# Kernel tuning notes

Measured on AMD Instinct MI355X. Metric: run time of the kernel, lower is better.

The kernel has to match this reference:

```python
import jax, jax.numpy as jnp
import numpy as np

B, L, HP, H, W = 4, 32, 32, 64, 64
D, DFFN, MAXL = 32, 64, 128

def setup_inputs() -> dict:
    key = jax.random.key(0)
    ks = jax.random.split(key, 20)
    rn = lambda k, s, sc=0.1: jax.random.normal(k, s, jnp.float32) * sc
    return {
        'x': jax.random.normal(ks[0], (B, 2 * L * HP, H, W), jnp.float32),
        'in_proj_w': rn(ks[1], (D, 12)), 'in_proj_b': rn(ks[2], (D,)),
        'layer_emb': rn(ks[3], (MAXL, D)),
        'time_decay': rn(ks[4], (D,)), 'time_first': rn(ks[5], (D,)),
        'ln_tm_g': jnp.ones((D,)), 'ln_tm_b': jnp.zeros((D,)),
        'tm_r': rn(ks[6], (D, D)), 'tm_k': rn(ks[7], (D, D)),
        'tm_v': rn(ks[8], (D, D)), 'tm_out': rn(ks[9], (D, D)),
        'ln_cm_g': jnp.ones((D,)), 'ln_cm_b': jnp.zeros((D,)),
        'cm_k': rn(ks[10], (DFFN, D)), 'cm_v': rn(ks[11], (D, DFFN)), 'cm_r': rn(ks[12], (D, D)),
        'gate_w': rn(ks[13], (1, D)), 'gate_b': rn(ks[14], (1,)),
        'row_w': rn(ks[15], (H, D)), 'row_b': rn(ks[16], (H,)),
        'col_w': rn(ks[17], (W, D)), 'col_b': rn(ks[18], (W,)),
    }

def _ln(x, g, b, eps=1e-5):
    mu = x.mean(-1, keepdims=True)
    var = ((x - mu) ** 2).mean(-1, keepdims=True)
    return (x - mu) * jax.lax.rsqrt(var + eps) * g + b

def _stats(a, b):
    # a, b: [B, L, HP, H, W] -> [B, L, HP, 12]
    af = a.reshape(*a.shape[:-2], -1)
    bf = b.reshape(*b.shape[:-2], -1)
    hs = lambda f: jnp.stack([f.mean(-1), f.std(-1, ddof=1), f.min(-1), f.max(-1)], -1)
    d = af - bf
    dm = d.mean(-1, keepdims=True)
    ds = d.std(-1, ddof=1, keepdims=True)
    dl2 = jnp.linalg.norm(d, axis=-1, keepdims=True)
    na = jnp.maximum(jnp.linalg.norm(af, axis=-1), 1e-8)
    nb = jnp.maximum(jnp.linalg.norm(bf, axis=-1), 1e-8)
    cos = ((af * bf).sum(-1) / (na * nb))[..., None]
    return jnp.concatenate([hs(af), hs(bf), dm, ds, dl2, cos], -1)

def reference(x, in_proj_w, in_proj_b, layer_emb, time_decay, time_first,
              ln_tm_g, ln_tm_b, tm_r, tm_k, tm_v, tm_out,
              ln_cm_g, ln_cm_b, cm_k, cm_v, cm_r,
              gate_w, gate_b, row_w, row_b, col_w, col_b):
    n = L * HP
    a = x[:, :n].reshape(B, L, HP, H, W)
    b = x[:, n:].reshape(B, L, HP, H, W)
    stats = _stats(a, b)                                   # [B,L,HP,12]
    feat_in = jnp.einsum('blhs,ds->blhd', stats, in_proj_w) + in_proj_b \
        + layer_emb[:L][None, :, None, :]
    feat_in = jnp.transpose(feat_in, (1, 0, 2, 3))         # [L,B,HP,D]
    wdec = jnp.exp(time_decay)

    def step(state, f):
        aa, bb, pp = state
        xn = _ln(f, ln_tm_g, ln_tm_b)
        r = jax.nn.sigmoid(xn @ tm_r.T)
        k = xn @ tm_k.T
        v = xn @ tm_v.T
        ww = time_first + k
        p = jnp.maximum(pp, ww)
        e1 = jnp.exp(pp - p)
        e2 = jnp.exp(ww - p)
        wkv = (e1 * aa + e2 * v) / jnp.maximum(e1 * bb + e2, 1e-8)
        ww2 = pp - wdec
        p2 = jnp.maximum(ww2, k)
        e1b = jnp.exp(ww2 - p2)
        e2b = jnp.exp(k - p2)
        y = f + r * (wkv @ tm_out.T)
        xn2 = _ln(y, ln_cm_g, ln_cm_b)
        kk = jnp.square(jax.nn.relu(xn2 @ cm_k.T))
        y = y + jax.nn.sigmoid(xn2 @ cm_r.T) * (kk @ cm_v.T)
        return (e1b * aa + e2b * v, e1b * bb + e2b, p2), y

    z = jnp.zeros((B, HP, D), x.dtype)
    init = (z, z, jnp.full((B, HP, D), -1e30, x.dtype))
    _, feats = jax.lax.scan(step, init, feat_in)           # [L,B,HP,D]

    gate = feats @ gate_w.T + gate_b                       # [L,B,HP,1]
    row = feats @ row_w.T + row_b                          # [L,B,HP,H]
    col = feats @ col_w.T + col_b                          # [L,B,HP,W]
    mask = jax.nn.sigmoid(gate[..., None] + row[..., None] + col[..., None, :])
    aT = jnp.transpose(a, (1, 0, 2, 3, 4))
    bT = jnp.transpose(b, (1, 0, 2, 3, 4))
    merged = mask * aT + (1.0 - mask) * bT                 # [L,B,HP,H,W]
    mixed = jnp.transpose(merged, (1, 0, 2, 3, 4)).reshape(B, n, H, W)
    return mixed, jax.nn.sigmoid(gate).mean(), mask.mean()
```

## Files before the change

### kernel.cpp

```cpp
#include <hip/hip_runtime.h>
#include <math.h>


__device__ __forceinline__ float sigf(float v) { return 1.0f / (1.0f + __expf(-v)); }

__global__ __launch_bounds__(256) void k_stats(
    const float* __restrict__ x, const float* __restrict__ in_proj_w,
    const float* __restrict__ in_proj_b, const float* __restrict__ layer_emb,
    const float* __restrict__ ln_tm_g, const float* __restrict__ ln_tm_b,
    const float* __restrict__ tm_r, const float* __restrict__ tm_k,
    const float* __restrict__ tm_v,
    float* __restrict__ f_out, float* __restrict__ r_out,
    float* __restrict__ kv_out)
{
    __shared__ float red[4][9];
    __shared__ float tot[9];
    __shared__ __align__(16) float xn_s[32];
    const int bid = blockIdx.x;
    const int hp = bid & 31, l = (bid >> 5) & 31, bb = bid >> 10;
    const float4* pa = (const float4*)(x + (size_t)(bb * 2048 + l * 32 + hp) * 4096);
    const float4* pb = (const float4*)(x + (size_t)(bb * 2048 + 1024 + l * 32 + hp) * 4096);
    const int t = threadIdx.x;
    const int gidx = ((l * 4 + bb) * 32 + hp) * 32;

    float sa = 0.f, saa = 0.f, sb = 0.f, sbb = 0.f, sab = 0.f;
    float mna = 3.4e38f, mxa = -3.4e38f, mnb = 3.4e38f, mxb = -3.4e38f;
#pragma unroll
    for (int it = 0; it < 4; ++it) {
        float4 a4 = pa[t + it * 256];
        float4 b4 = pb[t + it * 256];
        sa  += a4.x + a4.y + a4.z + a4.w;
        sb  += b4.x + b4.y + b4.z + b4.w;
        saa += a4.x * a4.x + a4.y * a4.y + a4.z * a4.z + a4.w * a4.w;
        sbb += b4.x * b4.x + b4.y * b4.y + b4.z * b4.z + b4.w * b4.w;
        sab += a4.x * b4.x + a4.y * b4.y + a4.z * b4.z + a4.w * b4.w;
        mna = fminf(mna, fminf(fminf(a4.x, a4.y), fminf(a4.z, a4.w)));
        mxa = fmaxf(mxa, fmaxf(fmaxf(a4.x, a4.y), fmaxf(a4.z, a4.w)));
        mnb = fminf(mnb, fminf(fminf(b4.x, b4.y), fminf(b4.z, b4.w)));
        mxb = fmaxf(mxb, fmaxf(fmaxf(b4.x, b4.y), fmaxf(b4.z, b4.w)));
    }
#pragma unroll
    for (int m = 1; m < 64; m <<= 1) {
        sa  += __shfl_xor(sa, m);
        saa += __shfl_xor(saa, m);
        sb  += __shfl_xor(sb, m);
        sbb += __shfl_xor(sbb, m);
        sab += __shfl_xor(sab, m);
        mna = fminf(mna, __shfl_xor(mna, m));
        mxa = fmaxf(mxa, __shfl_xor(mxa, m));
        mnb = fminf(mnb, __shfl_xor(mnb, m));
        mxb = fmaxf(mxb, __shfl_xor(mxb, m));
    }
    const int lane = t & 63, wv = t >> 6;
    if (lane == 0) {
        red[wv][0] = sa;  red[wv][1] = saa; red[wv][2] = sb;  red[wv][3] = sbb;
        red[wv][4] = sab; red[wv][5] = mna; red[wv][6] = mxa; red[wv][7] = mnb;
        red[wv][8] = mxb;
    }
    __syncthreads();
    if (t == 0) {
#pragma unroll
        for (int q = 0; q < 5; ++q) tot[q] = red[0][q] + red[1][q] + red[2][q] + red[3][q];
        tot[5] = fminf(fminf(red[0][5], red[1][5]), fminf(red[2][5], red[3][5]));
        tot[6] = fmaxf(fmaxf(red[0][6], red[1][6]), fmaxf(red[2][6], red[3][6]));
        tot[7] = fminf(fminf(red[0][7], red[1][7]), fminf(red[2][7], red[3][7]));
        tot[8] = fmaxf(fmaxf(red[0][8], red[1][8]), fmaxf(red[2][8], red[3][8]));
    }
    __syncthreads();
    if (t < 32) {
        const float SA = tot[0], SAA = tot[1], SB = tot[2], SBB = tot[3], SAB = tot[4];
        const float inv_n = 1.f / 4096.f, inv_nm1 = 1.f / 4095.f;
        float st[12];
        st[0] = SA * inv_n;
        st[1] = sqrtf(fmaxf(SAA - SA * SA * inv_n, 0.f) * inv_nm1);
        st[2] = tot[5]; st[3] = tot[6];
        st[4] = SB * inv_n;
        st[5] = sqrtf(fmaxf(SBB - SB * SB * inv_n, 0.f) * inv_nm1);
        st[6] = tot[7]; st[7] = tot[8];
        const float SD = SA - SB, SDD = SAA - 2.f * SAB + SBB;
        st[8]  = SD * inv_n;
        st[9]  = sqrtf(fmaxf(SDD - SD * SD * inv_n, 0.f) * inv_nm1);
        st[10] = sqrtf(fmaxf(SDD, 0.f));
        const float na = fmaxf(sqrtf(SAA), 1e-8f), nb2 = fmaxf(sqrtf(SBB), 1e-8f);
        st[11] = SAB / (na * nb2);
        float fv = in_proj_b[t] + layer_emb[l * 32 + t];
#pragma unroll
        for (int s2 = 0; s2 < 12; ++s2) fv += st[s2] * in_proj_w[t * 12 + s2];
        f_out[gidx + t] = fv;
        float s = fv, q = fv * fv;
#pragma unroll
        for (int m = 1; m < 32; m <<= 1) { s += __shfl_xor(s, m, 32); q += __shfl_xor(q, m, 32); }
        const float mu = s * (1.f / 32.f);
        const float var = fmaxf(q * (1.f / 32.f) - mu * mu, 0.f);
        xn_s[t] = (fv - mu) * rsqrtf(var + 1e-5f) * ln_tm_g[t] + ln_tm_b[t];
    }
    __syncthreads();
    if (t < 96) {
        const int d = t & 31;
        const float* wrow = (t < 32 ? tm_r : (t < 64 ? tm_k : tm_v)) + d * 32;
        const float4* w4 = (const float4*)wrow;
        const float4* x4 = (const float4*)xn_s;
        float a0 = 0.f, a1 = 0.f, a2 = 0.f, a3 = 0.f;
#pragma unroll
        for (int jq = 0; jq < 2; ++jq) {
            float4 w, xv;
            w = w4[jq];     xv = x4[jq];     a0 += w.x*xv.x + w.y*xv.y + w.z*xv.z + w.w*xv.w;
            w = w4[jq + 2]; xv = x4[jq + 2]; a1 += w.x*xv.x + w.y*xv.y + w.z*xv.z + w.w*xv.w;
            w = w4[jq + 4]; xv = x4[jq + 4]; a2 += w.x*xv.x + w.y*xv.y + w.z*xv.z + w.w*xv.w;
            w = w4[jq + 6]; xv = x4[jq + 6]; a3 += w.x*xv.x + w.y*xv.y + w.z*xv.z + w.w*xv.w;
        }
        const float dot = (a0 + a1) + (a2 + a3);
        if (t < 32)      r_out[gidx + d] = sigf(dot);
        else if (t < 64) kv_out[2 * (gidx + d)] = dot;
        else             kv_out[2 * (gidx + d) + 1] = dot;
    }
}

__global__ __launch_bounds__(64) void k_wkv(
    const float* __restrict__ kv_in,
    const float* __restrict__ time_decay, const float* __restrict__ time_first,
    float* __restrict__ wkv_out)
{
    const int ch = blockIdx.x * 64 + threadIdx.x;
    const int d = ch & 31;
    const float tf = time_first[d];
    const float wd = __expf(time_decay[d]);
    const float2* kv2 = (const float2*)kv_in;
    float2 kv[32];
#pragma unroll
    for (int l = 0; l < 32; ++l) kv[l] = kv2[l * 4096 + ch];
    float aa = 0.f, bbs = 0.f, pp = -1e30f;
#pragma unroll
    for (int l = 0; l < 32; ++l) {
        const float kc = kv[l].x, vc = kv[l].y;
        const float ww = tf + kc;
        const float p = fmaxf(pp, ww);
        const float e1 = __expf(pp - p), e2 = __expf(ww - p);
        wkv_out[l * 4096 + ch] = (e1 * aa + e2 * vc) / fmaxf(e1 * bbs + e2, 1e-8f);
        const float ww2 = pp - wd;
        const float p2 = fmaxf(ww2, kc);
        const float e1b = __expf(ww2 - p2), e2b = __expf(kc - p2);
        aa = e1b * aa + e2b * vc;
        bbs = e1b * bbs + e2b;
        pp = p2;
    }
}

__global__ __launch_bounds__(256) void k_merge(
    const float* __restrict__ x,
    const float* __restrict__ f_in, const float* __restrict__ r_in,
    const float* __restrict__ wkv_in,
    const float* __restrict__ tm_out,
    const float* __restrict__ ln_cm_g, const float* __restrict__ ln_cm_b,
    const float* __restrict__ cm_k, const float* __restrict__ cm_v,
    const float* __restrict__ cm_r,
    const float* __restrict__ gate_w, const float* __restrict__ gate_b,
    const float* __restrict__ row_w, const float* __restrict__ row_b,
    const float* __restrict__ col_w, const float* __restrict__ col_b,
    float* __restrict__ out, float* __restrict__ gpart, float* __restrict__ mpart)
{
    __shared__ __align__(16) float wkv_s[32];
    __shared__ __align__(16) float xn2_s[32];
    __shared__ __align__(16) float kk_s[64];
    __shared__ __align__(16) float fs[32];
    __shared__ float row_s[64], col_s[64];
    __shared__ float gate_sh;
    __shared__ float red2[4];
    const int bid = blockIdx.x;
    const int hp = bid & 31, l = (bid >> 5) & 31, bb = bid >> 10;
    const int t = threadIdx.x;
    const int gidx = ((l * 4 + bb) * 32 + hp) * 32;

    const float4* pa = (const float4*)(x + (size_t)(bb * 2048 + l * 32 + hp) * 4096);
    const float4* pb = (const float4*)(x + (size_t)(bb * 2048 + 1024 + l * 32 + hp) * 4096);
    float4* po = (float4*)(out + (size_t)(bb * 1024 + l * 32 + hp) * 4096);

    float4 av[4], bv[4];
#pragma unroll
    for (int it = 0; it < 4; ++it) {
        av[it] = pa[t + it * 256];
        bv[it] = pb[t + it * 256];
    }

    if (t < 64) {
        float yv = 0.f, y2 = 0.f;
        if (t < 32) {
            wkv_s[t] = wkv_in[gidx + t];
            const float fv = f_in[gidx + t];
            const float rv = r_in[gidx + t];
            const float4* w4 = (const float4*)(tm_out + t * 32);
            const float4* x4 = (const float4*)wkv_s;
            float a0 = 0.f, a1 = 0.f, a2 = 0.f, a3 = 0.f;
#pragma unroll
            for (int jq = 0; jq < 2; ++jq) {
                float4 w, xv;
                w = w4[jq];     xv = x4[jq];     a0 += w.x*xv.x + w.y*xv.y + w.z*xv.z + w.w*xv.w;
                w = w4[jq + 2]; xv = x4[jq + 2]; a1 += w.x*xv.x + w.y*xv.y + w.z*xv.z + w.w*xv.w;
                w = w4[jq + 4]; xv = x4[jq + 4]; a2 += w.x*xv.x + w.y*xv.y + w.z*xv.z + w.w*xv.w;
                w = w4[jq + 6]; xv = x4[jq + 6]; a3 += w.x*xv.x + w.y*xv.y + w.z*xv.z + w.w*xv.w;
            }
            yv = fv + rv * ((a0 + a1) + (a2 + a3));
            float s = yv, q = yv * yv;
#pragma unroll
            for (int m = 1; m < 32; m <<= 1) { s += __shfl_xor(s, m, 32); q += __shfl_xor(q, m, 32); }
            const float mu = s * (1.f / 32.f);
            const float var = fmaxf(q * (1.f / 32.f) - mu * mu, 0.f);
            xn2_s[t] = (yv - mu) * rsqrtf(var + 1e-5f) * ln_cm_g[t] + ln_cm_b[t];
        }
        {
            const float4* w4 = (const float4*)(cm_k + t * 32);
            const float4* x4 = (const float4*)xn2_s;
            float a0 = 0.f, a1 = 0.f, a2 = 0.f, a3 = 0.f;
#pragma unroll
            for (int jq = 0; jq < 2; ++jq) {
                float4 w, xv;
                w = w4[jq];     xv = x4[jq];     a0 += w.x*xv.x + w.y*xv.y + w.z*xv.z + w.w*xv.w;
                w = w4[jq + 2]; xv = x4[jq + 2]; a1 += w.x*xv.x + w.y*xv.y + w.z*xv.z + w.w*xv.w;
                w = w4[jq + 4]; xv = x4[jq + 4]; a2 += w.x*xv.x + w.y*xv.y + w.z*xv.z + w.w*xv.w;
                w = w4[jq + 6]; xv = x4[jq + 6]; a3 += w.x*xv.x + w.y*xv.y + w.z*xv.z + w.w*xv.w;
            }
            float kk = fmaxf((a0 + a1) + (a2 + a3), 0.f);
            kk_s[t] = kk * kk;
        }
        if (t < 32) {
            float cr;
            {
                const float4* w4 = (const float4*)(cm_r + t * 32);
                const float4* x4 = (const float4*)xn2_s;
                float a0 = 0.f, a1 = 0.f, a2 = 0.f, a3 = 0.f;
#pragma unroll
                for (int jq = 0; jq < 2; ++jq) {
                    float4 w, xv;
                    w = w4[jq];     xv = x4[jq];     a0 += w.x*xv.x + w.y*xv.y + w.z*xv.z + w.w*xv.w;
                    w = w4[jq + 2]; xv = x4[jq + 2]; a1 += w.x*xv.x + w.y*xv.y + w.z*xv.z + w.w*xv.w;
                    w = w4[jq + 4]; xv = x4[jq + 4]; a2 += w.x*xv.x + w.y*xv.y + w.z*xv.z + w.w*xv.w;
                    w = w4[jq + 6]; xv = x4[jq + 6]; a3 += w.x*xv.x + w.y*xv.y + w.z*xv.z + w.w*xv.w;
                }
                cr = sigf((a0 + a1) + (a2 + a3));
            }
            {
                const float4* w4 = (const float4*)(cm_v + t * 64);
                const float4* x4 = (const float4*)kk_s;
                float a0 = 0.f, a1 = 0.f, a2 = 0.f, a3 = 0.f;
#pragma unroll
                for (int jq = 0; jq < 4; ++jq) {
                    float4 w, xv;
                    w = w4[jq];      xv = x4[jq];      a0 += w.x*xv.x + w.y*xv.y + w.z*xv.z + w.w*xv.w;
                    w = w4[jq + 4];  xv = x4[jq + 4];  a1 += w.x*xv.x + w.y*xv.y + w.z*xv.z + w.w*xv.w;
                    w = w4[jq + 8];  xv = x4[jq + 8];  a2 += w.x*xv.x + w.y*xv.y + w.z*xv.z + w.w*xv.w;
                    w = w4[jq + 12]; xv = x4[jq + 12]; a3 += w.x*xv.x + w.y*xv.y + w.z*xv.z + w.w*xv.w;
                }
                y2 = yv + cr * ((a0 + a1) + (a2 + a3));
            }
            fs[t] = y2;
            float g = y2 * gate_w[t];
#pragma unroll
            for (int m = 1; m < 32; m <<= 1) g += __shfl_xor(g, m, 32);
            if (t == 0) gate_sh = g + gate_b[0];
        }
        {
            float a0 = row_b[t], a1 = 0.f, a2 = 0.f, a3 = 0.f;
            float c0 = col_b[t], c1 = 0.f, c2 = 0.f, c3 = 0.f;
#pragma unroll
            for (int d2 = 0; d2 < 8; ++d2) {
                const float f0 = fs[d2], f1 = fs[d2 + 8], f2 = fs[d2 + 16], f3 = fs[d2 + 24];
                a0 += f0 * row_w[t * 32 + d2];
                a1 += f1 * row_w[t * 32 + d2 + 8];
                a2 += f2 * row_w[t * 32 + d2 + 16];
                a3 += f3 * row_w[t * 32 + d2 + 24];
                c0 += f0 * col_w[t * 32 + d2];
                c1 += f1 * col_w[t * 32 + d2 + 8];
                c2 += f2 * col_w[t * 32 + d2 + 16];
                c3 += f3 * col_w[t * 32 + d2 + 24];
            }
            row_s[t] = (a0 + a1) + (a2 + a3);
            col_s[t] = (c0 + c1) + (c2 + c3);
        }
    }
    __syncthreads();

    const float gate = gate_sh;
    float msum = 0.f;
#pragma unroll
    for (int it = 0; it < 4; ++it) {
        const int i = t + it * 256;
        const float4 a4 = av[it];
        const float4 b4 = bv[it];
        const int h = i >> 4, w0 = (i & 15) * 4;
        const float gr = gate + row_s[h];
        const float m0 = sigf(gr + col_s[w0 + 0]);
        const float m1 = sigf(gr + col_s[w0 + 1]);
        const float m2 = sigf(gr + col_s[w0 + 2]);
        const float m3 = sigf(gr + col_s[w0 + 3]);
        float4 o;
        o.x = b4.x + m0 * (a4.x - b4.x);
        o.y = b4.y + m1 * (a4.y - b4.y);
        o.z = b4.z + m2 * (a4.z - b4.z);
        o.w = b4.w + m3 * (a4.w - b4.w);
        po[i] = o;
        msum += m0 + m1 + m2 + m3;
    }
#pragma unroll
    for (int m = 1; m < 64; m <<= 1) msum += __shfl_xor(msum, m);
    if ((t & 63) == 0) red2[t >> 6] = msum;
    __syncthreads();
    if (t == 0) {
        mpart[bid] = red2[0] + red2[1] + red2[2] + red2[3];
        gpart[bid] = sigf(gate);
    }
}

__global__ __launch_bounds__(256) void k_final(
    const float* __restrict__ gpart, const float* __restrict__ mpart,
    float* __restrict__ out)
{
    __shared__ float rg[4], rm[4];
    const int t = threadIdx.x;
    float gs = 0.f, ms = 0.f;
    for (int i = t; i < 4096; i += 256) { gs += gpart[i]; ms += mpart[i]; }
#pragma unroll
    for (int m = 1; m < 64; m <<= 1) { gs += __shfl_xor(gs, m); ms += __shfl_xor(ms, m); }
    if ((t & 63) == 0) { rg[t >> 6] = gs; rm[t >> 6] = ms; }
    __syncthreads();
    if (t == 0) {
        out[16777216] = (rg[0] + rg[1] + rg[2] + rg[3]) * (1.f / 4096.f);
        out[16777217] = (rm[0] + rm[1] + rm[2] + rm[3]) * (1.f / 16777216.f);
    }
}

extern "C" void kernel_launch(void* const* d_in, const int* in_sizes, int n_in,
                              void* d_out, int out_size, void* d_ws, size_t ws_size,
                              hipStream_t stream) {
    const float* x          = (const float*)d_in[0];
    const float* in_proj_w  = (const float*)d_in[1];
    const float* in_proj_b  = (const float*)d_in[2];
    const float* layer_emb  = (const float*)d_in[3];
    const float* time_decay = (const float*)d_in[4];
    const float* time_first = (const float*)d_in[5];
    const float* ln_tm_g    = (const float*)d_in[6];
    const float* ln_tm_b    = (const float*)d_in[7];
    const float* tm_r       = (const float*)d_in[8];
    const float* tm_k       = (const float*)d_in[9];
    const float* tm_v       = (const float*)d_in[10];
    const float* tm_out     = (const float*)d_in[11];
    const float* ln_cm_g    = (const float*)d_in[12];
    const float* ln_cm_b    = (const float*)d_in[13];
    const float* cm_k       = (const float*)d_in[14];
    const float* cm_v       = (const float*)d_in[15];
    const float* cm_r       = (const float*)d_in[16];
    const float* gate_w     = (const float*)d_in[17];
    const float* gate_b     = (const float*)d_in[18];
    const float* row_w      = (const float*)d_in[19];
    const float* row_b      = (const float*)d_in[20];
    const float* col_w      = (const float*)d_in[21];
    const float* col_b      = (const float*)d_in[22];
    float* out = (float*)d_out;

    float* wsf    = (float*)d_ws;
    float* f_ws   = wsf;
    float* r_ws   = wsf + 131072;
    float* kv_ws  = wsf + 262144;
    float* wkv_ws = wsf + 524288;
    float* gpart  = wsf + 655360;
    float* mpart  = wsf + 659456;

    k_stats<<<dim3(4096), dim3(256), 0, stream>>>(
        x, in_proj_w, in_proj_b, layer_emb, ln_tm_g, ln_tm_b,
        tm_r, tm_k, tm_v, f_ws, r_ws, kv_ws);
    k_wkv<<<dim3(64), dim3(64), 0, stream>>>(
        kv_ws, time_decay, time_first, wkv_ws);
    k_merge<<<dim3(4096), dim3(256), 0, stream>>>(
        x, f_ws, r_ws, wkv_ws, tm_out, ln_cm_g, ln_cm_b, cm_k, cm_v, cm_r,
        gate_w, gate_b, row_w, row_b, col_w, col_b, out, gpart, mpart);
    k_final<<<dim3(1), dim3(256), 0, stream>>>(gpart, mpart, out);
}
```

Baseline: 307.4 us.

## Drop a barrier in stats epilogue, add occupancy hints, defer merge loads

```diff
diff --git a/kernel.cpp b/kernel.cpp
--- a/kernel.cpp
+++ b/kernel.cpp
@@ -4,7 +4,7 @@
 
 __device__ __forceinline__ float sigf(float v) { return 1.0f / (1.0f + __expf(-v)); }
 
-__global__ __launch_bounds__(256) void k_stats(
+__global__ __launch_bounds__(256, 4) void k_stats(
     const float* __restrict__ x, const float* __restrict__ in_proj_w,
     const float* __restrict__ in_proj_b, const float* __restrict__ layer_emb,
     const float* __restrict__ ln_tm_g, const float* __restrict__ ln_tm_b,
@@ -14,7 +14,6 @@
     float* __restrict__ kv_out)
 {
     __shared__ float red[4][9];
-    __shared__ float tot[9];
     __shared__ __align__(16) float xn_s[32];
     const int bid = blockIdx.x;
     const int hp = bid & 31, l = (bid >> 5) & 31, bb = bid >> 10;
@@ -58,61 +57,71 @@
         red[wv][8] = mxb;
     }
     __syncthreads();
-    if (t == 0) {
-#pragma unroll
-        for (int q = 0; q < 5; ++q) tot[q] = red[0][q] + red[1][q] + red[2][q] + red[3][q];
-        tot[5] = fminf(fminf(red[0][5], red[1][5]), fminf(red[2][5], red[3][5]));
-        tot[6] = fmaxf(fmaxf(red[0][6], red[1][6]), fmaxf(red[2][6], red[3][6]));
-        tot[7] = fminf(fminf(red[0][7], red[1][7]), fminf(red[2][7], red[3][7]));
-        tot[8] = fmaxf(fmaxf(red[0][8], red[1][8]), fmaxf(red[2][8], red[3][8]));
-    }
-    __syncthreads();
-    if (t < 32) {
-        const float SA = tot[0], SAA = tot[1], SB = tot[2], SBB = tot[3], SAB = tot[4];
-        const float inv_n = 1.f / 4096.f, inv_nm1 = 1.f / 4095.f;
-        float st[12];
-        st[0] = SA * inv_n;
-        st[1] = sqrtf(fmaxf(SAA - SA * SA * inv_n, 0.f) * inv_nm1);
-        st[2] = tot[5]; st[3] = tot[6];
-        st[4] = SB * inv_n;
-        st[5] = sqrtf(fmaxf(SBB - SB * SB * inv_n, 0.f) * inv_nm1);
-        st[6] = tot[7]; st[7] = tot[8];
-        const float SD = SA - SB, SDD = SAA - 2.f * SAB + SBB;
-        st[8]  = SD * inv_n;
-        st[9]  = sqrtf(fmaxf(SDD - SD * SD * inv_n, 0.f) * inv_nm1);
-        st[10] = sqrtf(fmaxf(SDD, 0.f));
-        const float na = fmaxf(sqrtf(SAA), 1e-8f), nb2 = fmaxf(sqrtf(SBB), 1e-8f);
-        st[11] = SAB / (na * nb2);
-        float fv = in_proj_b[t] + layer_emb[l * 32 + t];
-#pragma unroll
-        for (int s2 = 0; s2 < 12; ++s2) fv += st[s2] * in_proj_w[t * 12 + s2];
-        f_out[gidx + t] = fv;
-        float s = fv, q = fv * fv;
-#pragma unroll
-        for (int m = 1; m < 32; m <<= 1) { s += __shfl_xor(s, m, 32); q += __shfl_xor(q, m, 32); }
-        const float mu = s * (1.f / 32.f);
-        const float var = fmaxf(q * (1.f / 32.f) - mu * mu, 0.f);
-        xn_s[t] = (fv - mu) * rsqrtf(var + 1e-5f) * ln_tm_g[t] + ln_tm_b[t];
-    }
-    __syncthreads();
-    if (t < 96) {
+    if (t < 64) {
+        if (t < 32) {
+            const float SA  = red[0][0] + red[1][0] + red[2][0] + red[3][0];
+            const float SAA = red[0][1] + red[1][1] + red[2][1] + red[3][1];
+            const float SB  = red[0][2] + red[1][2] + red[2][2] + red[3][2];
+            const float SBB = red[0][3] + red[1][3] + red[2][3] + red[3][3];
+            const float SAB = red[0][4] + red[1][4] + red[2][4] + red[3][4];
+            const float MNA = fminf(fminf(red[0][5], red[1][5]), fminf(red[2][5], red[3][5]));
+            const float MXA = fmaxf(fmaxf(red[0][6], red[1][6]), fmaxf(red[2][6], red[3][6]));
+            const float MNB = fminf(fminf(red[0][7], red[1][7]), fminf(red[2][7], red[3][7]));
+            const float MXB = fmaxf(fmaxf(red[0][8], red[1][8]), fmaxf(red[2][8], red[3][8]));
+            const float inv_n = 1.f / 4096.f, inv_nm1 = 1.f / 4095.f;
+            float st[12];
+            st[0] = SA * inv_n;
+            st[1] = sqrtf(fmaxf(SAA - SA * SA * inv_n, 0.f) * inv_nm1);
+            st[2] = MNA; st[3] = MXA;
+            st[4] = SB * inv_n;
+            st[5] = sqrtf(fmaxf(SBB - SB * SB * inv_n, 0.f) * inv_nm1);
+            st[6] = MNB; st[7] = MXB;
+            const float SD = SA - SB, SDD = SAA - 2.f * SAB + SBB;
+            st[8]  = SD * inv_n;
+            st[9]  = sqrtf(fmaxf(SDD - SD * SD * inv_n, 0.f) * inv_nm1);
+            st[10] = sqrtf(fmaxf(SDD, 0.f));
+            const float na = fmaxf(sqrtf(SAA), 1e-8f), nb2 = fmaxf(sqrtf(SBB), 1e-8f);
+            st[11] = SAB / (na * nb2);
+            float fv = in_proj_b[t] + layer_emb[l * 32 + t];
+#pragma unroll
+            for (int s2 = 0; s2 < 12; ++s2) fv += st[s2] * in_proj_w[t * 12 + s2];
+            f_out[gidx + t] = fv;
+            float s = fv, q = fv * fv;
+#pragma unroll
+            for (int m = 1; m < 32; m <<= 1) { s += __shfl_xor(s, m, 32); q += __shfl_xor(q, m, 32); }
+            const float mu = s * (1.f / 32.f);
+            const float var = fmaxf(q * (1.f / 32.f) - mu * mu, 0.f);
+            xn_s[t] = (fv - mu) * rsqrtf(var + 1e-5f) * ln_tm_g[t] + ln_tm_b[t];
+        }
         const int d = t & 31;
-        const float* wrow = (t < 32 ? tm_r : (t < 64 ? tm_k : tm_v)) + d * 32;
-        const float4* w4 = (const float4*)wrow;
         const float4* x4 = (const float4*)xn_s;
+        const float4* w1 = (const float4*)((t < 32 ? tm_r : tm_k) + d * 32);
         float a0 = 0.f, a1 = 0.f, a2 = 0.f, a3 = 0.f;
 #pragma unroll
         for (int jq = 0; jq < 2; ++jq) {
             float4 w, xv;
-            w = w4[jq];     xv = x4[jq];     a0 += w.x*xv.x + w.y*xv.y + w.z*xv.z + w.w*xv.w;
-            w = w4[jq + 2]; xv = x4[jq + 2]; a1 += w.x*xv.x + w.y*xv.y + w.z*xv.z + w.w*xv.w;
-            w = w4[jq + 4]; xv = x4[jq + 4]; a2 += w.x*xv.x + w.y*xv.y + w.z*xv.z + w.w*xv.w;
-            w = w4[jq + 6]; xv = x4[jq + 6]; a3 += w.x*xv.x + w.y*xv.y + w.z*xv.z + w.w*xv.w;
-        }
-        const float dot = (a0 + a1) + (a2 + a3);
-        if (t < 32)      r_out[gidx + d] = sigf(dot);
-        else if (t < 64) kv_out[2 * (gidx + d)] = dot;
-        else             kv_out[2 * (gidx + d) + 1] = dot;
+            w = w1[jq];     xv = x4[jq];     a0 += w.x*xv.x + w.y*xv.y + w.z*xv.z + w.w*xv.w;
+            w = w1[jq + 2]; xv = x4[jq + 2]; a1 += w.x*xv.x + w.y*xv.y + w.z*xv.z + w.w*xv.w;
+            w = w1[jq + 4]; xv = x4[jq + 4]; a2 += w.x*xv.x + w.y*xv.y + w.z*xv.z + w.w*xv.w;
+            w = w1[jq + 6]; xv = x4[jq + 6]; a3 += w.x*xv.x + w.y*xv.y + w.z*xv.z + w.w*xv.w;
+        }
+        const float dot1 = (a0 + a1) + (a2 + a3);
+        if (t < 32) {
+            r_out[gidx + d] = sigf(dot1);
+            const float4* w2 = (const float4*)(tm_v + d * 32);
+            float b0 = 0.f, b1 = 0.f, b2 = 0.f, b3 = 0.f;
+#pragma unroll
+            for (int jq = 0; jq < 2; ++jq) {
+                float4 w, xv;
+                w = w2[jq];     xv = x4[jq];     b0 += w.x*xv.x + w.y*xv.y + w.z*xv.z + w.w*xv.w;
+                w = w2[jq + 2]; xv = x4[jq + 2]; b1 += w.x*xv.x + w.y*xv.y + w.z*xv.z + w.w*xv.w;
+                w = w2[jq + 4]; xv = x4[jq + 4]; b2 += w.x*xv.x + w.y*xv.y + w.z*xv.z + w.w*xv.w;
+                w = w2[jq + 6]; xv = x4[jq + 6]; b3 += w.x*xv.x + w.y*xv.y + w.z*xv.z + w.w*xv.w;
+            }
+            kv_out[2 * (gidx + d) + 1] = (b0 + b1) + (b2 + b3);
+        } else {
+            kv_out[2 * (gidx + d)] = dot1;
+        }
     }
 }
 
@@ -146,7 +155,7 @@
     }
 }
 
-__global__ __launch_bounds__(256) void k_merge(
+__global__ __launch_bounds__(256, 4) void k_merge(
     const float* __restrict__ x,
     const float* __restrict__ f_in, const float* __restrict__ r_in,
     const float* __restrict__ wkv_in,
@@ -175,13 +184,6 @@
     const float4* pb = (const float4*)(x + (size_t)(bb * 2048 + 1024 + l * 32 + hp) * 4096);
     float4* po = (float4*)(out + (size_t)(bb * 1024 + l * 32 + hp) * 4096);
 
-    float4 av[4], bv[4];
-#pragma unroll
-    for (int it = 0; it < 4; ++it) {
-        av[it] = pa[t + it * 256];
-        bv[it] = pb[t + it * 256];
-    }
-
     if (t < 64) {
         float yv = 0.f, y2 = 0.f;
         if (t < 32) {
@@ -284,8 +286,8 @@
 #pragma unroll
     for (int it = 0; it < 4; ++it) {
         const int i = t + it * 256;
-        const float4 a4 = av[it];
-        const float4 b4 = bv[it];
+        const float4 a4 = pa[i];
+        const float4 b4 = pb[i];
         const int h = i >> 4, w0 = (i & 15) * 4;
         const float gr = gate + row_s[h];
         const float m0 = sigf(gr + col_s[w0 + 0]);
```

New measurement: 300.9 us. 2.1% less time.
